# Performance work log

Measured on AMD Instinct MI355X. Metric: run time of the kernel, lower is better.

Reference implementation:

```python
import jax, jax.numpy as jnp
import numpy as np

# dims: F sparse fields, vocab V, embed E, batch B, ND dense feats, D domains,
# H bottom hidden (bottom_params dims=[128]), T tower hidden (tower_params dims=[8])
F, V, E = 26, 100000, 16
B, ND, D = 16384, 13, 4
H, T = 128, 8
IN = F * E + ND


def setup_inputs() -> dict:
    key = jax.random.key(0)
    ks = jax.random.split(key, 10)
    return {
        "sparse_ids": jax.random.randint(ks[0], (B, F), 0, V, dtype=jnp.int32),
        "dense": jax.random.normal(ks[1], (B, ND), dtype=jnp.float32),
        "domain_id": jax.random.randint(ks[2], (B,), 0, D, dtype=jnp.int32),
        "emb_tables": jax.random.normal(ks[3], (F, V, E), dtype=jnp.float32) * 0.05,
        "W_bottom": jax.random.normal(ks[4], (IN, H), dtype=jnp.float32) * 0.05,
        "b_bottom": jnp.zeros((H,), dtype=jnp.float32),
        "tower_W1": jax.random.normal(ks[5], (D, H, T), dtype=jnp.float32) * 0.1,
        "tower_b1": jnp.zeros((D, T), dtype=jnp.float32),
        "tower_W2": jax.random.normal(ks[6], (D, T), dtype=jnp.float32) * 0.1,
        "tower_b2": jnp.zeros((D,), dtype=jnp.float32),
    }


def reference(sparse_ids, dense, domain_id, emb_tables, W_bottom, b_bottom,
              tower_W1, tower_b1, tower_W2, tower_b2):
    # per-field embedding lookup: [B, F, E]
    emb = jax.vmap(lambda tbl, idx: tbl[idx], in_axes=(0, 1), out_axes=1)(emb_tables, sparse_ids)
    # squeeze_dim=True -> concat flattened embeddings with dense features: [B, F*E + ND]
    x = jnp.concatenate([emb.reshape(emb.shape[0], -1), dense], axis=-1)
    # shared bottom MLP (dims=[128], relu)
    feat = jax.nn.relu(x @ W_bottom + b_bottom)  # [B, H]
    # per-domain tower: gather each row's tower params by domain id (MoE-style dispatch,
    # same math as the masked gather/scatter loop in the original)
    w1 = tower_W1[domain_id]                         # [B, H, T]
    h = jax.nn.relu(jnp.einsum('bh,bht->bt', feat, w1) + tower_b1[domain_id])  # [B, T]
    logit = jnp.einsum('bt,bt->b', h, tower_W2[domain_id]) + tower_b2[domain_id]
    # aux_logit is zeros in this path
    return jax.nn.sigmoid(logit)  # [B]
```

## Files before the change

### kernel.cpp

```cpp
#include <hip/hip_runtime.h>
#include <math.h>

#define F_  26
#define V_  100000
#define E_  16
#define B_  16384
#define ND_ 13
#define D_  4
#define H_  128
#define T_  8
#define KP  448
#define NKS 14
#define XSTR 456
#define FSTR 136
#define BB  32
#define NT  512
#define NGT 7

typedef short bf16x8 __attribute__((ext_vector_type(8)));
typedef float f32x4  __attribute__((ext_vector_type(4)));

__device__ __forceinline__ unsigned short f2bf(float f) {
    unsigned int u = __float_as_uint(f);
    u += 0x7FFF + ((u >> 16) & 1);
    return (unsigned short)(u >> 16);
}

__global__ __launch_bounds__(256)
void prep_kernel(const float* __restrict__ W_bottom,
                 const float* __restrict__ tower_W1,
                 unsigned short* __restrict__ wsB,
                 unsigned short* __restrict__ wsT1)
{
    const int tid = blockIdx.x * 256 + threadIdx.x;
    if (tid < NKS * 8 * 64) {
        const int s   = tid >> 9;
        const int rem = tid & 511;
        const int n   = rem >> 6;
        const int l   = rem & 63;
        const int kbase = s * 32 + ((l >> 4) << 3);
        const int col   = (n << 4) + (l & 15);
        unsigned long long lo = 0, hi = 0;
#pragma unroll
        for (int j = 0; j < 4; ++j) {
            const int k = kbase + j;
            const float f = (k < 429) ? W_bottom[k * H_ + col] : 0.f;
            lo |= (unsigned long long)f2bf(f) << (16 * j);
        }
#pragma unroll
        for (int j = 0; j < 4; ++j) {
            const int k = kbase + 4 + j;
            const float f = (k < 429) ? W_bottom[k * H_ + col] : 0.f;
            hi |= (unsigned long long)f2bf(f) << (16 * j);
        }
        ulonglong2 pack; pack.x = lo; pack.y = hi;
        *reinterpret_cast<ulonglong2*>(wsB + (size_t)tid * 8) = pack;
    } else {
        const int t2 = tid - NKS * 8 * 64;
        if (t2 < 8 * 64) {
            const int frag = t2 >> 6;
            const int l    = t2 & 63;
            const int ks2  = frag >> 1;
            const int n2   = frag & 1;
            const int kbase = ks2 * 32 + ((l >> 4) << 3);
            const int col   = (n2 << 4) + (l & 15);
            const int d     = col >> 3;
            const int tt    = col & 7;
            unsigned long long lo = 0, hi = 0;
#pragma unroll
            for (int j = 0; j < 4; ++j) {
                const int h = kbase + j;
                lo |= (unsigned long long)f2bf(tower_W1[((d << 7) + h) * T_ + tt]) << (16 * j);
            }
#pragma unroll
            for (int j = 0; j < 4; ++j) {
                const int h = kbase + 4 + j;
                hi |= (unsigned long long)f2bf(tower_W1[((d << 7) + h) * T_ + tt]) << (16 * j);
            }
            ulonglong2 pack; pack.x = lo; pack.y = hi;
            *reinterpret_cast<ulonglong2*>(wsT1 + (size_t)t2 * 8) = pack;
        }
    }
}

__global__ __launch_bounds__(NT, 4)
void sb_fused_kernel(const int* __restrict__ sparse_ids,
                     const float* __restrict__ dense,
                     const int* __restrict__ domain_id,
                     const float* __restrict__ emb_tables,
                     const float* __restrict__ b_bottom,
                     const float* __restrict__ tower_b1,
                     const float* __restrict__ tower_W2,
                     const float* __restrict__ tower_b2,
                     const unsigned short* __restrict__ wsB,
                     const unsigned short* __restrict__ wsT1,
                     float* __restrict__ out)
{
    __shared__ unsigned short x_lds[BB][XSTR];
    __shared__ unsigned short feat_lds[BB][FSTR];

    const int t  = threadIdx.x;
    const int r0 = blockIdx.x * BB;

    {
        int    ldsoff[NGT];
        int    id_[NGT];
        int    fq_[NGT];
        float4 v_[NGT];
#pragma unroll
        for (int it = 0; it < NGT; ++it) {
            const int idx = t + (it << 9);
            if (idx < BB * F_ * 4) {
                const int q   = idx & 3;
                const int rf  = idx >> 2;
                const int row = rf / F_;
                const int f   = rf - row * F_;
                id_[it]    = sparse_ids[(r0 + row) * F_ + f];
                fq_[it]    = (f << 2) | q;
                ldsoff[it] = row * XSTR + (f << 4) + (q << 2);
            }
        }
#pragma unroll
        for (int it = 0; it < NGT; ++it) {
            const int idx = t + (it << 9);
            if (idx < BB * F_ * 4) {
                const int f = fq_[it] >> 2;
                const int q = fq_[it] & 3;
                v_[it] = *reinterpret_cast<const float4*>(
                    emb_tables + ((size_t)f * V_ + (size_t)id_[it]) * E_ + (q << 2));
            }
        }
#pragma unroll
        for (int it = 0; it < NGT; ++it) {
            const int idx = t + (it << 9);
            if (idx < BB * F_ * 4) {
                ushort4 b;
                b.x = f2bf(v_[it].x); b.y = f2bf(v_[it].y);
                b.z = f2bf(v_[it].z); b.w = f2bf(v_[it].w);
                *reinterpret_cast<ushort4*>(&x_lds[0][0] + ldsoff[it]) = b;
            }
        }
    }
#pragma unroll
    for (int it = 0; it < 2; ++it) {
        const int idx = t + (it << 9);
        const int row = idx >> 5;
        const int c   = 416 + (idx & 31);
        x_lds[row][c] = (c < 429) ? f2bf(dense[(r0 + row) * ND_ + (c - 416)]) : 0;
    }
    __syncthreads();

    const int l   = t & 63;
    const int w   = t >> 6;
    const int lhi = l >> 4;
    const int llo = l & 15;

    f32x4 acc0 = {0.f,0.f,0.f,0.f};
    f32x4 acc1 = acc0;

    const bf16x8* wsBv = reinterpret_cast<const bf16x8*>(wsB);
#pragma unroll 2
    for (int ks = 0; ks < NKS; ++ks) {
        const int ko = ks * 32 + (lhi << 3);
        const bf16x8 a0 = *reinterpret_cast<const bf16x8*>(&x_lds[llo][ko]);
        const bf16x8 a1 = *reinterpret_cast<const bf16x8*>(&x_lds[16 + llo][ko]);
        const bf16x8 b  = wsBv[((ks << 3) + w) * 64 + l];
        acc0 = __builtin_amdgcn_mfma_f32_16x16x32_bf16(a0, b, acc0, 0, 0, 0);
        acc1 = __builtin_amdgcn_mfma_f32_16x16x32_bf16(a1, b, acc1, 0, 0, 0);
    }

    {
        const int c = (w << 4) + llo;
        const float bias = b_bottom[c];
#pragma unroll
        for (int i = 0; i < 4; ++i) {
            const int r = (lhi << 2) + i;
            feat_lds[r][c]      = f2bf(fmaxf(acc0[i] + bias, 0.f));
            feat_lds[16 + r][c] = f2bf(fmaxf(acc1[i] + bias, 0.f));
        }
    }
    __syncthreads();

    if (w < 4) {
        const int mt = w >> 1;
        const int nt = w & 1;
        f32x4 acc = {0.f,0.f,0.f,0.f};
        const bf16x8* wsT1v = reinterpret_cast<const bf16x8*>(wsT1);
#pragma unroll
        for (int ks2 = 0; ks2 < 4; ++ks2) {
            const bf16x8 a = *reinterpret_cast<const bf16x8*>(
                &feat_lds[(mt << 4) + llo][(ks2 << 5) + (lhi << 3)]);
            const bf16x8 b = wsT1v[((ks2 << 1) + nt) * 64 + l];
            acc = __builtin_amdgcn_mfma_f32_16x16x32_bf16(a, b, acc, 0, 0, 0);
        }
        const int col    = (nt << 4) + llo;
        const float b1v  = tower_b1[col];
        const float w2v  = tower_W2[col];
        const int  dlane = (nt << 1) + (llo >> 3);
        const bool writer = ((llo & 7) == 0);
#pragma unroll
        for (int i = 0; i < 4; ++i) {
            float v = fmaxf(acc[i] + b1v, 0.f) * w2v;
            v += __shfl_xor(v, 1);
            v += __shfl_xor(v, 2);
            v += __shfl_xor(v, 4);
            if (writer) {
                const int r   = (mt << 4) + (lhi << 2) + i;
                const int d_r = domain_id[r0 + r];
                if (d_r == dlane) {
                    out[r0 + r] = 1.f / (1.f + expf(-(v + tower_b2[d_r])));
                }
            }
        }
    }
}

extern "C" void kernel_launch(void* const* d_in, const int* in_sizes, int n_in,
                              void* d_out, int out_size, void* d_ws, size_t ws_size,
                              hipStream_t stream) {
    const int*   sparse_ids = (const int*)  d_in[0];
    const float* dense      = (const float*)d_in[1];
    const int*   domain_id  = (const int*)  d_in[2];
    const float* emb_tables = (const float*)d_in[3];
    const float* W_bottom   = (const float*)d_in[4];
    const float* b_bottom   = (const float*)d_in[5];
    const float* tower_W1   = (const float*)d_in[6];
    const float* tower_b1   = (const float*)d_in[7];
    const float* tower_W2   = (const float*)d_in[8];
    const float* tower_b2   = (const float*)d_in[9];
    float* out = (float*)d_out;

    unsigned short* wsB  = (unsigned short*)d_ws;
    unsigned short* wsT1 = (unsigned short*)((char*)d_ws + 131072);

    prep_kernel<<<(NKS * 8 * 64 + 8 * 64 + 255) / 256, 256, 0, stream>>>(
        W_bottom, tower_W1, wsB, wsT1);

    sb_fused_kernel<<<B_ / BB, NT, 0, stream>>>(
        sparse_ids, dense, domain_id, emb_tables,
        b_bottom, tower_b1, tower_W2, tower_b2, wsB, wsT1, out);
}
```

Measured before the change: 25.48 us.

## Fuse weight bf16 packing into main kernel and drop prep launch

Removes the separate prep kernel that converted W_bottom and tower_W1 into MFMA-fragment bf16 layout. Each thread of the fused kernel now loads its own weight fragments directly from fp32 global memory into registers before the embedding gather, overlapping those loads with the gather latency. This saves one kernel launch and a workspace round trip. The cost is redundant weight loads and conversions in every block (512 blocks) and much higher register pressure from holding 14 B-fragments.

```diff
diff --git a/kernel.cpp b/kernel.cpp
--- a/kernel.cpp
+++ b/kernel.cpp
@@ -9,13 +9,11 @@
 #define D_  4
 #define H_  128
 #define T_  8
-#define KP  448
 #define NKS 14
 #define XSTR 456
 #define FSTR 136
 #define BB  32
 #define NT  512
-#define NGT 7
 
 typedef short bf16x8 __attribute__((ext_vector_type(8)));
 typedef float f32x4  __attribute__((ext_vector_type(4)));
@@ -26,74 +24,19 @@
     return (unsigned short)(u >> 16);
 }
 
-__global__ __launch_bounds__(256)
-void prep_kernel(const float* __restrict__ W_bottom,
-                 const float* __restrict__ tower_W1,
-                 unsigned short* __restrict__ wsB,
-                 unsigned short* __restrict__ wsT1)
-{
-    const int tid = blockIdx.x * 256 + threadIdx.x;
-    if (tid < NKS * 8 * 64) {
-        const int s   = tid >> 9;
-        const int rem = tid & 511;
-        const int n   = rem >> 6;
-        const int l   = rem & 63;
-        const int kbase = s * 32 + ((l >> 4) << 3);
-        const int col   = (n << 4) + (l & 15);
-        unsigned long long lo = 0, hi = 0;
-#pragma unroll
-        for (int j = 0; j < 4; ++j) {
-            const int k = kbase + j;
-            const float f = (k < 429) ? W_bottom[k * H_ + col] : 0.f;
-            lo |= (unsigned long long)f2bf(f) << (16 * j);
-        }
-#pragma unroll
-        for (int j = 0; j < 4; ++j) {
-            const int k = kbase + 4 + j;
-            const float f = (k < 429) ? W_bottom[k * H_ + col] : 0.f;
-            hi |= (unsigned long long)f2bf(f) << (16 * j);
-        }
-        ulonglong2 pack; pack.x = lo; pack.y = hi;
-        *reinterpret_cast<ulonglong2*>(wsB + (size_t)tid * 8) = pack;
-    } else {
-        const int t2 = tid - NKS * 8 * 64;
-        if (t2 < 8 * 64) {
-            const int frag = t2 >> 6;
-            const int l    = t2 & 63;
-            const int ks2  = frag >> 1;
-            const int n2   = frag & 1;
-            const int kbase = ks2 * 32 + ((l >> 4) << 3);
-            const int col   = (n2 << 4) + (l & 15);
-            const int d     = col >> 3;
-            const int tt    = col & 7;
-            unsigned long long lo = 0, hi = 0;
-#pragma unroll
-            for (int j = 0; j < 4; ++j) {
-                const int h = kbase + j;
-                lo |= (unsigned long long)f2bf(tower_W1[((d << 7) + h) * T_ + tt]) << (16 * j);
-            }
-#pragma unroll
-            for (int j = 0; j < 4; ++j) {
-                const int h = kbase + 4 + j;
-                hi |= (unsigned long long)f2bf(tower_W1[((d << 7) + h) * T_ + tt]) << (16 * j);
-            }
-            ulonglong2 pack; pack.x = lo; pack.y = hi;
-            *reinterpret_cast<ulonglong2*>(wsT1 + (size_t)t2 * 8) = pack;
-        }
-    }
-}
+union BF8 { bf16x8 v; unsigned short us[8]; };
 
 __global__ __launch_bounds__(NT, 4)
 void sb_fused_kernel(const int* __restrict__ sparse_ids,
                      const float* __restrict__ dense,
                      const int* __restrict__ domain_id,
                      const float* __restrict__ emb_tables,
+                     const float* __restrict__ W_bottom,
                      const float* __restrict__ b_bottom,
+                     const float* __restrict__ tower_W1,
                      const float* __restrict__ tower_b1,
                      const float* __restrict__ tower_W2,
                      const float* __restrict__ tower_b2,
-                     const unsigned short* __restrict__ wsB,
-                     const unsigned short* __restrict__ wsT1,
                      float* __restrict__ out)
 {
     __shared__ unsigned short x_lds[BB][XSTR];
@@ -101,43 +44,104 @@
 
     const int t  = threadIdx.x;
     const int r0 = blockIdx.x * BB;
+    const int l   = t & 63;
+    const int w   = t >> 6;
+    const int lhi = l >> 4;
+    const int llo = l & 15;
+
+    int id_[7];
+#pragma unroll
+    for (int it = 0; it < 7; ++it) {
+        const int idx = t + (it << 9);
+        if (it < 6 || idx < BB * F_ * 4) {
+            const int rf  = idx >> 2;
+            const int row = rf / F_;
+            const int f   = rf - row * F_;
+            id_[it] = sparse_ids[(r0 + row) * F_ + f];
+        }
+    }
+
+    const int c = (w << 4) + llo;
+    bf16x8 bfrag[NKS];
+#pragma unroll
+    for (int ks = 0; ks < NKS; ++ks) {
+        const int rbase = (ks << 5) + (lhi << 3);
+        BF8 u;
+#pragma unroll
+        for (int j = 0; j < 8; ++j) {
+            const int r = rbase + j;
+            const float f = (r < 429) ? W_bottom[(r << 7) + c] : 0.f;
+            u.us[j] = f2bf(f);
+        }
+        bfrag[ks] = u.v;
+    }
+
+    bf16x8 tfrag[4];
+    if (w < 4) {
+        const int ct = ((w & 1) << 4) + llo;
+        const int d  = ct >> 3;
+        const int tt = ct & 7;
+#pragma unroll
+        for (int ks2 = 0; ks2 < 4; ++ks2) {
+            const int hbase = (ks2 << 5) + (lhi << 3);
+            BF8 u;
+#pragma unroll
+            for (int j = 0; j < 8; ++j) {
+                u.us[j] = f2bf(tower_W1[(d << 10) + ((hbase + j) << 3) + tt]);
+            }
+            tfrag[ks2] = u.v;
+        }
+    }
 
     {
-        int    ldsoff[NGT];
-        int    id_[NGT];
-        int    fq_[NGT];
-        float4 v_[NGT];
-#pragma unroll
-        for (int it = 0; it < NGT; ++it) {
-            const int idx = t + (it << 9);
-            if (idx < BB * F_ * 4) {
+        float4 va[4];
+#pragma unroll
+        for (int it = 0; it < 4; ++it) {
+            const int idx = t + (it << 9);
+            const int q   = idx & 3;
+            const int rf  = idx >> 2;
+            const int row = rf / F_;
+            const int f   = rf - row * F_;
+            va[it] = *reinterpret_cast<const float4*>(
+                emb_tables + ((size_t)f * V_ + (size_t)id_[it]) * E_ + (q << 2));
+        }
+        float4 vb[3];
+#pragma unroll
+        for (int it = 4; it < 7; ++it) {
+            const int idx = t + (it << 9);
+            if (it < 6 || idx < BB * F_ * 4) {
                 const int q   = idx & 3;
                 const int rf  = idx >> 2;
                 const int row = rf / F_;
                 const int f   = rf - row * F_;
-                id_[it]    = sparse_ids[(r0 + row) * F_ + f];
-                fq_[it]    = (f << 2) | q;
-                ldsoff[it] = row * XSTR + (f << 4) + (q << 2);
-            }
-        }
-#pragma unroll
-        for (int it = 0; it < NGT; ++it) {
-            const int idx = t + (it << 9);
-            if (idx < BB * F_ * 4) {
-                const int f = fq_[it] >> 2;
-                const int q = fq_[it] & 3;
-                v_[it] = *reinterpret_cast<const float4*>(
+                vb[it - 4] = *reinterpret_cast<const float4*>(
                     emb_tables + ((size_t)f * V_ + (size_t)id_[it]) * E_ + (q << 2));
             }
         }
 #pragma unroll
-        for (int it = 0; it < NGT; ++it) {
-            const int idx = t + (it << 9);
-            if (idx < BB * F_ * 4) {
+        for (int it = 0; it < 4; ++it) {
+            const int idx = t + (it << 9);
+            const int q   = idx & 3;
+            const int rf  = idx >> 2;
+            const int row = rf / F_;
+            const int f   = rf - row * F_;
+            ushort4 b;
+            b.x = f2bf(va[it].x); b.y = f2bf(va[it].y);
+            b.z = f2bf(va[it].z); b.w = f2bf(va[it].w);
+            *reinterpret_cast<ushort4*>(&x_lds[row][(f << 4) + (q << 2)]) = b;
+        }
+#pragma unroll
+        for (int it = 4; it < 7; ++it) {
+            const int idx = t + (it << 9);
+            if (it < 6 || idx < BB * F_ * 4) {
+                const int q   = idx & 3;
+                const int rf  = idx >> 2;
+                const int row = rf / F_;
+                const int f   = rf - row * F_;
                 ushort4 b;
-                b.x = f2bf(v_[it].x); b.y = f2bf(v_[it].y);
-                b.z = f2bf(v_[it].z); b.w = f2bf(v_[it].w);
-                *reinterpret_cast<ushort4*>(&x_lds[0][0] + ldsoff[it]) = b;
+                b.x = f2bf(vb[it - 4].x); b.y = f2bf(vb[it - 4].y);
+                b.z = f2bf(vb[it - 4].z); b.w = f2bf(vb[it - 4].w);
+                *reinterpret_cast<ushort4*>(&x_lds[row][(f << 4) + (q << 2)]) = b;
             }
         }
     }
@@ -145,32 +149,24 @@
     for (int it = 0; it < 2; ++it) {
         const int idx = t + (it << 9);
         const int row = idx >> 5;
-        const int c   = 416 + (idx & 31);
-        x_lds[row][c] = (c < 429) ? f2bf(dense[(r0 + row) * ND_ + (c - 416)]) : 0;
+        const int cc  = 416 + (idx & 31);
+        x_lds[row][cc] = (cc < 429) ? f2bf(dense[(r0 + row) * ND_ + (cc - 416)]) : 0;
     }
     __syncthreads();
-
-    const int l   = t & 63;
-    const int w   = t >> 6;
-    const int lhi = l >> 4;
-    const int llo = l & 15;
 
     f32x4 acc0 = {0.f,0.f,0.f,0.f};
     f32x4 acc1 = acc0;
 
-    const bf16x8* wsBv = reinterpret_cast<const bf16x8*>(wsB);
-#pragma unroll 2
+#pragma unroll
     for (int ks = 0; ks < NKS; ++ks) {
-        const int ko = ks * 32 + (lhi << 3);
+        const int ko = (ks << 5) + (lhi << 3);
         const bf16x8 a0 = *reinterpret_cast<const bf16x8*>(&x_lds[llo][ko]);
         const bf16x8 a1 = *reinterpret_cast<const bf16x8*>(&x_lds[16 + llo][ko]);
-        const bf16x8 b  = wsBv[((ks << 3) + w) * 64 + l];
-        acc0 = __builtin_amdgcn_mfma_f32_16x16x32_bf16(a0, b, acc0, 0, 0, 0);
-        acc1 = __builtin_amdgcn_mfma_f32_16x16x32_bf16(a1, b, acc1, 0, 0, 0);
+        acc0 = __builtin_amdgcn_mfma_f32_16x16x32_bf16(a0, bfrag[ks], acc0, 0, 0, 0);
+        acc1 = __builtin_amdgcn_mfma_f32_16x16x32_bf16(a1, bfrag[ks], acc1, 0, 0, 0);
     }
 
     {
-        const int c = (w << 4) + llo;
         const float bias = b_bottom[c];
 #pragma unroll
         for (int i = 0; i < 4; ++i) {
@@ -185,13 +181,11 @@
         const int mt = w >> 1;
         const int nt = w & 1;
         f32x4 acc = {0.f,0.f,0.f,0.f};
-        const bf16x8* wsT1v = reinterpret_cast<const bf16x8*>(wsT1);
 #pragma unroll
         for (int ks2 = 0; ks2 < 4; ++ks2) {
             const bf16x8 a = *reinterpret_cast<const bf16x8*>(
                 &feat_lds[(mt << 4) + llo][(ks2 << 5) + (lhi << 3)]);
-            const bf16x8 b = wsT1v[((ks2 << 1) + nt) * 64 + l];
-            acc = __builtin_amdgcn_mfma_f32_16x16x32_bf16(a, b, acc, 0, 0, 0);
+            acc = __builtin_amdgcn_mfma_f32_16x16x32_bf16(a, tfrag[ks2], acc, 0, 0, 0);
         }
         const int col    = (nt << 4) + llo;
         const float b1v  = tower_b1[col];
@@ -230,13 +224,7 @@
     const float* tower_b2   = (const float*)d_in[9];
     float* out = (float*)d_out;
 
-    unsigned short* wsB  = (unsigned short*)d_ws;
-    unsigned short* wsT1 = (unsigned short*)((char*)d_ws + 131072);
-
-    prep_kernel<<<(NKS * 8 * 64 + 8 * 64 + 255) / 256, 256, 0, stream>>>(
-        W_bottom, tower_W1, wsB, wsT1);
-
     sb_fused_kernel<<<B_ / BB, NT, 0, stream>>>(
         sparse_ids, dense, domain_id, emb_tables,
-        b_bottom, tower_b1, tower_W2, tower_b2, wsB, wsT1, out);
+        W_bottom, b_bottom, tower_W1, tower_b1, tower_W2, tower_b2, out);
 }
```

Result: slower. 42.01 us (+64.9%).
